# Optimization experiments

Measured on AMD Instinct MI355X. Metric: run time of the kernel, lower is better.

## Reference

```python
import jax, jax.numpy as jnp
import numpy as np

EPS = 1e-6

def _grad_magnitude(x):
    # x: [B, 1, D, H, W]. Valid 3x3x3 conv with shift-subtract kernels:
    # kernel_w differences along D, kernel_d along H, kernel_h along W.
    g_w = x[:, :, 2:, 1:-1, 1:-1] - x[:, :, :-2, 1:-1, 1:-1]
    g_d = x[:, :, 1:-1, 2:, 1:-1] - x[:, :, 1:-1, :-2, 1:-1]
    g_h = x[:, :, 1:-1, 1:-1, 2:] - x[:, :, 1:-1, 1:-1, :-2]
    mag = jnp.sqrt(g_w * g_w + g_d * g_d + g_h * g_h + EPS)
    # replicate-pad back to original spatial size
    return jnp.pad(mag, ((0, 0), (0, 0), (1, 1), (1, 1), (1, 1)), mode='edge')

def setup_inputs() -> dict:
    key = jax.random.key(0)
    k1, k2 = jax.random.split(key)
    shape = (1, 1, 256, 256, 256)
    x1 = jax.random.normal(k1, shape, dtype=jnp.float32)
    x2 = jax.random.normal(k2, shape, dtype=jnp.float32)
    return {"x1": x1, "x2": x2}

def reference(x1, x2):
    g1 = _grad_magnitude(x1)
    g2 = _grad_magnitude(x2)
    return jnp.mean(jnp.abs(g1 - g2))
```

## Files before the change

kernel.cpp:

```cpp
#include <hip/hip_runtime.h>


#define D_CHUNK 4

__global__ __launch_bounds__(256) void grad_loss_kernel(const float* __restrict__ xf1,
                                                        const float* __restrict__ xf2,
                                                        double* __restrict__ acc) {
    const float4* __restrict__ x1 = (const float4*)xf1;
    const float4* __restrict__ x2 = (const float4*)xf2;

    __shared__ float4 plane[2][2][6][64];

    const int tid   = threadIdx.x;
    const int lane  = tid & 63;
    const int wid   = tid >> 6;
    const int htile = blockIdx.x & 63;
    const int dchk  = blockIdx.x >> 6;

    const int h0 = 1 + htile * 4;
    const int d0 = 1 + dchk * D_CHUNK;

    const int  h    = h0 + wid;
    const bool live = (h <= 254);
    const int  hrow = (h <= 255) ? h : 255;

    const int halo_row  = (wid < 2) ? (h0 - 1) : ((h0 + 4 <= 255) ? (h0 + 4) : 255);
    const int halo_slot = (wid < 2) ? 0 : 5;
    const int halo_inp  = wid & 1;
    const float4* __restrict__ halo4 = halo_inp ? x2 : x1;

    const int own_f4  = hrow * 64 + lane;
    const int halo_f4 = halo_row * 64 + lane;

    const float ww0 = (lane == 0)  ? 0.0f : 1.0f;
    const float ww1 = (lane == 0)  ? 2.0f : 1.0f;
    const float ww2 = (lane == 63) ? 2.0f : 1.0f;
    const float ww3 = (lane == 63) ? 0.0f : 1.0f;
    const float whf = (h == 1 || h == 254) ? 2.0f : 1.0f;

    float4 a1 = x1[(d0 - 1) * 16384 + own_f4];
    float4 a2 = x2[(d0 - 1) * 16384 + own_f4];
    float4 b1 = x1[d0 * 16384 + own_f4];
    float4 b2 = x2[d0 * 16384 + own_f4];
    float4 hb = halo4[d0 * 16384 + halo_f4];
    float4 c1 = x1[(d0 + 1) * 16384 + own_f4];
    float4 c2 = x2[(d0 + 1) * 16384 + own_f4];
    float4 hc = halo4[(d0 + 1) * 16384 + halo_f4];

    plane[0][0][wid + 1][lane] = b1;
    plane[0][1][wid + 1][lane] = b2;
    plane[0][halo_inp][halo_slot][lane] = hb;
    __syncthreads();

    float val = 0.0f;

    #pragma unroll
    for (int i = 0; i < D_CHUNK; ++i) {
        const int d   = d0 + i;
        const int cur = i & 1;
        const int nxt = cur ^ 1;
        const int dn  = (d + 2 <= 255) ? (d + 2) : 255;

        float4 n1 = x1[dn * 16384 + own_f4];
        float4 n2 = x2[dn * 16384 + own_f4];
        float4 hn = halo4[dn * 16384 + halo_f4];

        plane[nxt][0][wid + 1][lane] = c1;
        plane[nxt][1][wid + 1][lane] = c2;
        plane[nxt][halo_inp][halo_slot][lane] = hc;

        if (live && d <= 254) {
            float4 u1 = plane[cur][0][wid][lane];
            float4 v1 = plane[cur][0][wid + 2][lane];
            float4 u2 = plane[cur][1][wid][lane];
            float4 v2 = plane[cur][1][wid + 2][lane];

            float l1 = __shfl_up(b1.w, 1, 64);
            float r1 = __shfl_down(b1.x, 1, 64);
            float l2 = __shfl_up(b2.w, 1, 64);
            float r2 = __shfl_down(b2.x, 1, 64);

            float gw, gd, gh;
            gw = c1.x - a1.x; gd = v1.x - u1.x; gh = b1.y - l1;
            float m10 = __builtin_amdgcn_sqrtf(gw * gw + gd * gd + gh * gh + 1e-6f);
            gw = c1.y - a1.y; gd = v1.y - u1.y; gh = b1.z - b1.x;
            float m11 = __builtin_amdgcn_sqrtf(gw * gw + gd * gd + gh * gh + 1e-6f);
            gw = c1.z - a1.z; gd = v1.z - u1.z; gh = b1.w - b1.y;
            float m12 = __builtin_amdgcn_sqrtf(gw * gw + gd * gd + gh * gh + 1e-6f);
            gw = c1.w - a1.w; gd = v1.w - u1.w; gh = r1 - b1.z;
            float m13 = __builtin_amdgcn_sqrtf(gw * gw + gd * gd + gh * gh + 1e-6f);

            gw = c2.x - a2.x; gd = v2.x - u2.x; gh = b2.y - l2;
            float m20 = __builtin_amdgcn_sqrtf(gw * gw + gd * gd + gh * gh + 1e-6f);
            gw = c2.y - a2.y; gd = v2.y - u2.y; gh = b2.z - b2.x;
            float m21 = __builtin_amdgcn_sqrtf(gw * gw + gd * gd + gh * gh + 1e-6f);
            gw = c2.z - a2.z; gd = v2.z - u2.z; gh = b2.w - b2.y;
            float m22 = __builtin_amdgcn_sqrtf(gw * gw + gd * gd + gh * gh + 1e-6f);
            gw = c2.w - a2.w; gd = v2.w - u2.w; gh = r2 - b2.z;
            float m23 = __builtin_amdgcn_sqrtf(gw * gw + gd * gd + gh * gh + 1e-6f);

            float inner = ww0 * fabsf(m10 - m20)
                        + ww1 * fabsf(m11 - m21)
                        + ww2 * fabsf(m12 - m22)
                        + ww3 * fabsf(m13 - m23);

            const float wdf = (d == 1 || d == 254) ? 2.0f : 1.0f;
            val += wdf * whf * inner;
        }

        a1 = b1; b1 = c1; c1 = n1;
        a2 = b2; b2 = c2; c2 = n2;
        hc = hn;
        __syncthreads();
    }

    for (int off = 32; off > 0; off >>= 1)
        val += __shfl_down(val, off, 64);

    __shared__ float smem[4];
    if (lane == 0) smem[wid] = val;
    __syncthreads();

    if (wid == 0) {
        float s = (lane < 4) ? smem[lane] : 0.0f;
        s += __shfl_down(s, 2, 64);
        s += __shfl_down(s, 1, 64);
        if (lane == 0)
            atomicAdd(&acc[blockIdx.x & 255], (double)s);
    }
}

__global__ void finalize_kernel(const double* __restrict__ acc, float* __restrict__ out) {
    double v = acc[threadIdx.x];
    for (int off = 32; off > 0; off >>= 1)
        v += __shfl_down(v, off, 64);

    __shared__ double smem[4];
    const int lid = threadIdx.x & 63;
    const int wid = threadIdx.x >> 6;
    if (lid == 0) smem[wid] = v;
    __syncthreads();

    if (threadIdx.x == 0) {
        double s = smem[0] + smem[1] + smem[2] + smem[3];
        out[0] = (float)(s / 16777216.0);
    }
}

extern "C" void kernel_launch(void* const* d_in, const int* in_sizes, int n_in,
                              void* d_out, int out_size, void* d_ws, size_t ws_size,
                              hipStream_t stream) {
    const float* x1 = (const float*)d_in[0];
    const float* x2 = (const float*)d_in[1];
    float* out = (float*)d_out;
    double* acc = (double*)d_ws;

    hipMemsetAsync(d_ws, 0, 256 * sizeof(double), stream);
    grad_loss_kernel<<<64 * 64, 256, 0, stream>>>(x1, x2, acc);
    finalize_kernel<<<1, 256, 0, stream>>>(acc, out);
}
```

Measured before the change: 145.9 us.

## Replace LDS halo planes with direct per-wave neighbor-row loads and longer D chunks

```diff
diff --git a/kernel.cpp b/kernel.cpp
--- a/kernel.cpp
+++ b/kernel.cpp
@@ -1,102 +1,94 @@
 #include <hip/hip_runtime.h>
 
 
-#define D_CHUNK 4
+#define D_CHUNK 16
 
-__global__ __launch_bounds__(256) void grad_loss_kernel(const float* __restrict__ xf1,
-                                                        const float* __restrict__ xf2,
-                                                        double* __restrict__ acc) {
+__global__ __launch_bounds__(256, 4) void grad_loss_kernel(const float* __restrict__ xf1,
+                                                           const float* __restrict__ xf2,
+                                                           double* __restrict__ acc) {
     const float4* __restrict__ x1 = (const float4*)xf1;
     const float4* __restrict__ x2 = (const float4*)xf2;
 
-    __shared__ float4 plane[2][2][6][64];
+    const int tid  = threadIdx.x;
+    const int lane = tid & 63;
+    const int wid  = tid >> 6;
 
-    const int tid   = threadIdx.x;
-    const int lane  = tid & 63;
-    const int wid   = tid >> 6;
-    const int htile = blockIdx.x & 63;
-    const int dchk  = blockIdx.x >> 6;
+    const int orig = blockIdx.x;
+    const int wg   = (orig & 7) * 128 + (orig >> 3);
+    const int htile = wg & 63;
+    const int dchk  = wg >> 6;
 
-    const int h0 = 1 + htile * 4;
+    const int  r    = 1 + htile * 4 + wid;
+    const bool live = (r <= 254);
+    const int  rc   = (r <= 255) ? r : 255;
+    const int  rm   = r - 1;
+    const int  rp   = (r + 1 <= 255) ? (r + 1) : 255;
+
+    const int iU = rm * 64 + lane;
+    const int iC = rc * 64 + lane;
+    const int iV = rp * 64 + lane;
+
     const int d0 = 1 + dchk * D_CHUNK;
-
-    const int  h    = h0 + wid;
-    const bool live = (h <= 254);
-    const int  hrow = (h <= 255) ? h : 255;
-
-    const int halo_row  = (wid < 2) ? (h0 - 1) : ((h0 + 4 <= 255) ? (h0 + 4) : 255);
-    const int halo_slot = (wid < 2) ? 0 : 5;
-    const int halo_inp  = wid & 1;
-    const float4* __restrict__ halo4 = halo_inp ? x2 : x1;
-
-    const int own_f4  = hrow * 64 + lane;
-    const int halo_f4 = halo_row * 64 + lane;
 
     const float ww0 = (lane == 0)  ? 0.0f : 1.0f;
     const float ww1 = (lane == 0)  ? 2.0f : 1.0f;
     const float ww2 = (lane == 63) ? 2.0f : 1.0f;
     const float ww3 = (lane == 63) ? 0.0f : 1.0f;
-    const float whf = (h == 1 || h == 254) ? 2.0f : 1.0f;
+    const float whf = (r == 1 || r == 254) ? 2.0f : 1.0f;
 
-    float4 a1 = x1[(d0 - 1) * 16384 + own_f4];
-    float4 a2 = x2[(d0 - 1) * 16384 + own_f4];
-    float4 b1 = x1[d0 * 16384 + own_f4];
-    float4 b2 = x2[d0 * 16384 + own_f4];
-    float4 hb = halo4[d0 * 16384 + halo_f4];
-    float4 c1 = x1[(d0 + 1) * 16384 + own_f4];
-    float4 c2 = x2[(d0 + 1) * 16384 + own_f4];
-    float4 hc = halo4[(d0 + 1) * 16384 + halo_f4];
-
-    plane[0][0][wid + 1][lane] = b1;
-    plane[0][1][wid + 1][lane] = b2;
-    plane[0][halo_inp][halo_slot][lane] = hb;
-    __syncthreads();
+    float4 a1  = x1[(d0 - 1) * 16384 + iC];
+    float4 a2  = x2[(d0 - 1) * 16384 + iC];
+    float4 bU1 = x1[d0 * 16384 + iU];
+    float4 bC1 = x1[d0 * 16384 + iC];
+    float4 bV1 = x1[d0 * 16384 + iV];
+    float4 bU2 = x2[d0 * 16384 + iU];
+    float4 bC2 = x2[d0 * 16384 + iC];
+    float4 bV2 = x2[d0 * 16384 + iV];
+    float4 cU1 = x1[(d0 + 1) * 16384 + iU];
+    float4 cC1 = x1[(d0 + 1) * 16384 + iC];
+    float4 cV1 = x1[(d0 + 1) * 16384 + iV];
+    float4 cU2 = x2[(d0 + 1) * 16384 + iU];
+    float4 cC2 = x2[(d0 + 1) * 16384 + iC];
+    float4 cV2 = x2[(d0 + 1) * 16384 + iV];
 
     float val = 0.0f;
 
-    #pragma unroll
+    #pragma unroll 2
     for (int i = 0; i < D_CHUNK; ++i) {
-        const int d   = d0 + i;
-        const int cur = i & 1;
-        const int nxt = cur ^ 1;
-        const int dn  = (d + 2 <= 255) ? (d + 2) : 255;
+        const int d  = d0 + i;
+        const int dn = (d + 2 <= 255) ? (d + 2) : 255;
+        const int off = dn * 16384;
 
-        float4 n1 = x1[dn * 16384 + own_f4];
-        float4 n2 = x2[dn * 16384 + own_f4];
-        float4 hn = halo4[dn * 16384 + halo_f4];
-
-        plane[nxt][0][wid + 1][lane] = c1;
-        plane[nxt][1][wid + 1][lane] = c2;
-        plane[nxt][halo_inp][halo_slot][lane] = hc;
+        float4 qU1 = x1[off + iU];
+        float4 qC1 = x1[off + iC];
+        float4 qV1 = x1[off + iV];
+        float4 qU2 = x2[off + iU];
+        float4 qC2 = x2[off + iC];
+        float4 qV2 = x2[off + iV];
 
         if (live && d <= 254) {
-            float4 u1 = plane[cur][0][wid][lane];
-            float4 v1 = plane[cur][0][wid + 2][lane];
-            float4 u2 = plane[cur][1][wid][lane];
-            float4 v2 = plane[cur][1][wid + 2][lane];
-
-            float l1 = __shfl_up(b1.w, 1, 64);
-            float r1 = __shfl_down(b1.x, 1, 64);
-            float l2 = __shfl_up(b2.w, 1, 64);
-            float r2 = __shfl_down(b2.x, 1, 64);
+            float l1 = __shfl_up(bC1.w, 1, 64);
+            float r1 = __shfl_down(bC1.x, 1, 64);
+            float l2 = __shfl_up(bC2.w, 1, 64);
+            float r2 = __shfl_down(bC2.x, 1, 64);
 
             float gw, gd, gh;
-            gw = c1.x - a1.x; gd = v1.x - u1.x; gh = b1.y - l1;
+            gw = cC1.x - a1.x; gd = bV1.x - bU1.x; gh = bC1.y - l1;
             float m10 = __builtin_amdgcn_sqrtf(gw * gw + gd * gd + gh * gh + 1e-6f);
-            gw = c1.y - a1.y; gd = v1.y - u1.y; gh = b1.z - b1.x;
+            gw = cC1.y - a1.y; gd = bV1.y - bU1.y; gh = bC1.z - bC1.x;
             float m11 = __builtin_amdgcn_sqrtf(gw * gw + gd * gd + gh * gh + 1e-6f);
-            gw = c1.z - a1.z; gd = v1.z - u1.z; gh = b1.w - b1.y;
+            gw = cC1.z - a1.z; gd = bV1.z - bU1.z; gh = bC1.w - bC1.y;
             float m12 = __builtin_amdgcn_sqrtf(gw * gw + gd * gd + gh * gh + 1e-6f);
-            gw = c1.w - a1.w; gd = v1.w - u1.w; gh = r1 - b1.z;
+            gw = cC1.w - a1.w; gd = bV1.w - bU1.w; gh = r1 - bC1.z;
             float m13 = __builtin_amdgcn_sqrtf(gw * gw + gd * gd + gh * gh + 1e-6f);
 
-            gw = c2.x - a2.x; gd = v2.x - u2.x; gh = b2.y - l2;
+            gw = cC2.x - a2.x; gd = bV2.x - bU2.x; gh = bC2.y - l2;
             float m20 = __builtin_amdgcn_sqrtf(gw * gw + gd * gd + gh * gh + 1e-6f);
-            gw = c2.y - a2.y; gd = v2.y - u2.y; gh = b2.z - b2.x;
+            gw = cC2.y - a2.y; gd = bV2.y - bU2.y; gh = bC2.z - bC2.x;
             float m21 = __builtin_amdgcn_sqrtf(gw * gw + gd * gd + gh * gh + 1e-6f);
-            gw = c2.z - a2.z; gd = v2.z - u2.z; gh = b2.w - b2.y;
+            gw = cC2.z - a2.z; gd = bV2.z - bU2.z; gh = bC2.w - bC2.y;
             float m22 = __builtin_amdgcn_sqrtf(gw * gw + gd * gd + gh * gh + 1e-6f);
-            gw = c2.w - a2.w; gd = v2.w - u2.w; gh = r2 - b2.z;
+            gw = cC2.w - a2.w; gd = bV2.w - bU2.w; gh = r2 - bC2.z;
             float m23 = __builtin_amdgcn_sqrtf(gw * gw + gd * gd + gh * gh + 1e-6f);
 
             float inner = ww0 * fabsf(m10 - m20)
@@ -108,10 +100,8 @@
             val += wdf * whf * inner;
         }
 
-        a1 = b1; b1 = c1; c1 = n1;
-        a2 = b2; b2 = c2; c2 = n2;
-        hc = hn;
-        __syncthreads();
+        a1 = bC1; bU1 = cU1; bC1 = cC1; bV1 = cV1; cU1 = qU1; cC1 = qC1; cV1 = qV1;
+        a2 = bC2; bU2 = cU2; bC2 = cC2; bV2 = cV2; cU2 = qU2; cC2 = qC2; cV2 = qV2;
     }
 
     for (int off = 32; off > 0; off >>= 1)
@@ -156,6 +146,6 @@
     double* acc = (double*)d_ws;
 
     hipMemsetAsync(d_ws, 0, 256 * sizeof(double), stream);
-    grad_loss_kernel<<<64 * 64, 256, 0, stream>>>(x1, x2, acc);
+    grad_loss_kernel<<<64 * 16, 256, 0, stream>>>(x1, x2, acc);
     finalize_kernel<<<1, 256, 0, stream>>>(acc, out);
 }
```

Result: slower. 149.8 us (+2.7%).
